# Optimization experiments

Hardware: AMD Instinct MI355X
Metric: run time of the kernel (lower is better)

The kernel has to match this reference:

```python
import jax, jax.numpy as jnp
import numpy as np

B, N, C_IN, C_OUT, R_IN, R_OUT, NUM_PSI, E = 4, 1024, 128, 256, 32, 32, 2, 65536


def psi(x, src, dst, W, b):
    # GIN-style GNN layer: aggregate neighbors via scatter-add, then linear+relu
    agg = jax.ops.segment_sum(x[src], dst, num_segments=x.shape[0])
    return jax.nn.relu((x + agg) @ W + b)


def setup_inputs() -> dict:
    key = jax.random.key(0)
    ks = jax.random.split(key, 12)
    inp = {
        'x_s': jax.random.normal(ks[0], (B * N, C_IN), jnp.float32),
        'edge_index_s': jax.random.randint(ks[1], (2, E), 0, B * N, jnp.int32),
        'x_t': jax.random.normal(ks[2], (B * N, C_IN), jnp.float32),
        'edge_index_t': jax.random.randint(ks[3], (2, E), 0, B * N, jnp.int32),
        'r': jax.random.normal(ks[4], (NUM_PSI, B, N, R_IN), jnp.float32),
        'W1': jax.random.normal(ks[5], (C_IN, C_OUT), jnp.float32) * (0.2 / np.sqrt(C_IN)),
        'b1': jnp.zeros((C_OUT,), jnp.float32),
        'Wp': jax.random.normal(ks[6], (NUM_PSI, R_IN, R_OUT), jnp.float32) * (1.0 / np.sqrt(R_IN)),
        'bp': jnp.zeros((NUM_PSI, R_OUT), jnp.float32),
        'Wm1': jax.random.normal(ks[7], (R_OUT, R_OUT), jnp.float32) * (1.0 / np.sqrt(R_OUT)),
        'bm1': jnp.zeros((R_OUT,), jnp.float32),
        'Wm2': jax.random.normal(ks[8], (R_OUT, 1), jnp.float32) * (1.0 / np.sqrt(R_OUT)),
        'bm2': jnp.zeros((1,), jnp.float32),
        'sum_weights': jnp.ones((NUM_PSI + 1,), jnp.float32),
    }
    return inp


def reference(x_s, edge_index_s, x_t, edge_index_t, r, W1, b1, Wp, bp, Wm1, bm1, Wm2, bm2, sum_weights):
    src_s, dst_s = edge_index_s[0], edge_index_s[1]
    src_t, dst_t = edge_index_t[0], edge_index_t[1]
    # psi_1 node embeddings, then dense-batch (equal-size graphs -> masks all true)
    h_s = psi(x_s, src_s, dst_s, W1, b1).reshape(B, N, C_OUT)
    h_t = psi(x_t, src_t, dst_t, W1, b1).reshape(B, N, C_OUT)
    S_hat = jnp.einsum('bsc,btc->bst', h_s, h_t)  # [B, N_s, N_t]
    S_0 = jax.nn.softmax(S_hat, axis=-1)
    S_stack = []
    for i in range(NUM_PSI):  # structurally distinct psi modules
        S = jax.nn.softmax(S_hat, axis=-1)
        r_s = r[i]  # [B, N, R_IN] random node indicators
        r_t = jnp.einsum('bst,bsr->btr', S, r_s)
        o_s = psi(r_s.reshape(B * N, R_IN), src_s, dst_s, Wp[i], bp[i]).reshape(B, N, R_OUT)
        o_t = psi(r_t.reshape(B * N, R_IN), src_t, dst_t, Wp[i], bp[i]).reshape(B, N, R_OUT)
        D = o_s[:, :, None, :] - o_t[:, None, :, :]  # [B, N_s, N_t, R_OUT]
        upd = (jax.nn.relu(D @ Wm1 + bm1) @ Wm2 + bm2)[..., 0]
        S_hat = S_hat + upd
        S_stack.append(jax.nn.softmax(S_hat, axis=-1))
    S_final = sum_weights[0] * S_0
    for i in range(NUM_PSI):
        S_final = S_final + sum_weights[i + 1] * S_stack[i]
    return jax.nn.softmax(S_final.reshape(B * N, N), axis=-1)
```

## Files before the change

### kernel.cpp

```cpp
#include <hip/hip_runtime.h>
#include <hip/hip_bf16.h>

#define NBATCH 4
#define NSEQ   1024
#define BNN    4096
#define CIN    128
#define COUT   256
#define RDIM   32
#define NEDGE  65536

__global__ void edge_hist(const int* __restrict__ ei_s, const int* __restrict__ ei_t,
                          int* __restrict__ cnt) {
    int gid = blockIdx.x * blockDim.x + threadIdx.x;
    int list = gid >> 16;
    int e = gid & (NEDGE - 1);
    const int* ei = list ? ei_t : ei_s;
    atomicAdd(&cnt[list * BNN + ei[NEDGE + e]], 1);
}

__global__ void edge_scan(const int* __restrict__ cnt, int* __restrict__ offs,
                          int* __restrict__ cursor) {
    __shared__ int sums[256];
    int list = blockIdx.x;
    int tid = threadIdx.x;
    int local[16];
    int s = 0;
#pragma unroll
    for (int k = 0; k < 16; k++) { local[k] = cnt[list * BNN + tid * 16 + k]; s += local[k]; }
    sums[tid] = s;
    __syncthreads();
    for (int off = 1; off < 256; off <<= 1) {
        int v = 0;
        if (tid >= off) v = sums[tid - off];
        __syncthreads();
        if (tid >= off) sums[tid] += v;
        __syncthreads();
    }
    int run = tid ? sums[tid - 1] : 0;
#pragma unroll
    for (int k = 0; k < 16; k++) {
        offs[list * (BNN + 1) + tid * 16 + k] = run;
        cursor[list * BNN + tid * 16 + k] = run;
        run += local[k];
    }
    if (tid == 255) offs[list * (BNN + 1) + BNN] = run;
}

__global__ void edge_place(const int* __restrict__ ei_s, const int* __restrict__ ei_t,
                           int* __restrict__ cursor, int* __restrict__ ssrc) {
    int gid = blockIdx.x * blockDim.x + threadIdx.x;
    int list = gid >> 16;
    int e = gid & (NEDGE - 1);
    const int* ei = list ? ei_t : ei_s;
    int dst = ei[NEDGE + e], src = ei[e];
    int p = atomicAdd(&cursor[list * BNN + dst], 1);
    ssrc[list * NEDGE + p] = src;
}

__global__ void gather_agg128(const float* __restrict__ x_s, const float* __restrict__ x_t,
                              const int* __restrict__ offs, const int* __restrict__ ssrc,
                              float* __restrict__ t_s, float* __restrict__ t_t) {
    int node = blockIdx.x & (BNN - 1);
    int list = blockIdx.x >> 12;
    const float* x = list ? x_t : x_s;
    float* t = list ? t_t : t_s;
    int c = threadIdx.x;
    int beg = offs[list * (BNN + 1) + node], end = offs[list * (BNN + 1) + node + 1];
    float acc = x[(size_t)node * CIN + c];
    for (int e = beg; e < end; e++)
        acc += x[(size_t)ssrc[list * NEDGE + e] * CIN + c];
    t[(size_t)node * CIN + c] = acc;
}

__global__ void gather_agg32(const float* __restrict__ rs, const float* __restrict__ rtin,
                             const int* __restrict__ offs, const int* __restrict__ ssrc,
                             float* __restrict__ trs, float* __restrict__ trt) {
    int list = blockIdx.y;
    int node = blockIdx.x * 8 + (threadIdx.x >> 5);
    int c = threadIdx.x & 31;
    const float* in = list ? rtin : rs;
    float* outp = list ? trt : trs;
    int beg = offs[list * (BNN + 1) + node], end = offs[list * (BNN + 1) + node + 1];
    float acc = in[(size_t)node * RDIM + c];
    for (int e = beg; e < end; e++)
        acc += in[(size_t)ssrc[list * NEDGE + e] * RDIM + c];
    outp[(size_t)node * RDIM + c] = acc;
}

__global__ void psi1_gemm(const float* __restrict__ t, const float* __restrict__ W1,
                          const float* __restrict__ b1, float* __restrict__ h) {
    __shared__ float rows[8][CIN];
    int r0 = blockIdx.x * 8;
    int tid = threadIdx.x;
    {
        int rr = tid >> 5, c4 = (tid & 31) << 2;
        *(float4*)&rows[rr][c4] = *(const float4*)(t + (size_t)(r0 + rr) * CIN + c4);
    }
    __syncthreads();
    float acc[8];
    float bias = b1[tid];
#pragma unroll
    for (int r = 0; r < 8; r++) acc[r] = bias;
    for (int k = 0; k < CIN; k++) {
        float w = W1[k * COUT + tid];
#pragma unroll
        for (int r = 0; r < 8; r++) acc[r] = fmaf(rows[r][k], w, acc[r]);
    }
#pragma unroll
    for (int r = 0; r < 8; r++)
        h[(size_t)(r0 + r) * COUT + tid] = fmaxf(acc[r], 0.f);
}

__global__ void shat_gemm(const float* __restrict__ hs, const float* __restrict__ ht,
                          float* __restrict__ Sh) {
    __shared__ float As[32][68];
    __shared__ float Bs[32][68];
    int b  = blockIdx.z;
    int s0 = blockIdx.y * 64, t0 = blockIdx.x * 64;
    const float* A  = hs + (size_t)b * NSEQ * COUT;
    const float* Bm = ht + (size_t)b * NSEQ * COUT;
    int tid = threadIdx.x;
    int tx = tid & 15, ty = tid >> 4;
    float acc[4][4] = {};
    for (int k0 = 0; k0 < COUT; k0 += 32) {
#pragma unroll
        for (int q = 0; q < 2; q++) {
            int lid = (tid << 1) + q;
            int row = lid >> 3, k4 = (lid & 7) << 2;
            float4 av = *(const float4*)(A + (size_t)(s0 + row) * COUT + k0 + k4);
            As[k4 + 0][row] = av.x; As[k4 + 1][row] = av.y;
            As[k4 + 2][row] = av.z; As[k4 + 3][row] = av.w;
            float4 bv = *(const float4*)(Bm + (size_t)(t0 + row) * COUT + k0 + k4);
            Bs[k4 + 0][row] = bv.x; Bs[k4 + 1][row] = bv.y;
            Bs[k4 + 2][row] = bv.z; Bs[k4 + 3][row] = bv.w;
        }
        __syncthreads();
#pragma unroll
        for (int k = 0; k < 32; k++) {
            float av[4], bv[4];
#pragma unroll
            for (int i = 0; i < 4; i++) av[i] = As[k][ty * 4 + i];
#pragma unroll
            for (int j = 0; j < 4; j++) bv[j] = Bs[k][tx * 4 + j];
#pragma unroll
            for (int i = 0; i < 4; i++)
#pragma unroll
                for (int j = 0; j < 4; j++)
                    acc[i][j] = fmaf(av[i], bv[j], acc[i][j]);
        }
        __syncthreads();
    }
#pragma unroll
    for (int i = 0; i < 4; i++) {
        float4 v = make_float4(acc[i][0], acc[i][1], acc[i][2], acc[i][3]);
        *(float4*)(Sh + ((size_t)b * NSEQ + s0 + ty * 4 + i) * NSEQ + t0 + tx * 4) = v;
    }
}

__global__ void softmax_acc(const float* __restrict__ Sh, float* __restrict__ S,
                            float* __restrict__ Sfin, const float* __restrict__ sw,
                            int widx, int init) {
    int row = blockIdx.x, tid = threadIdx.x;
    float4 v = *(const float4*)(Sh + (size_t)row * NSEQ + tid * 4);
    float m = fmaxf(fmaxf(v.x, v.y), fmaxf(v.z, v.w));
#pragma unroll
    for (int o = 32; o; o >>= 1) m = fmaxf(m, __shfl_xor(m, o));
    __shared__ float redm[4], reds[4];
    int wid = tid >> 6, lane = tid & 63;
    if (lane == 0) redm[wid] = m;
    __syncthreads();
    m = fmaxf(fmaxf(redm[0], redm[1]), fmaxf(redm[2], redm[3]));
    float4 e;
    e.x = __expf(v.x - m); e.y = __expf(v.y - m);
    e.z = __expf(v.z - m); e.w = __expf(v.w - m);
    float s = e.x + e.y + e.z + e.w;
#pragma unroll
    for (int o = 32; o; o >>= 1) s += __shfl_xor(s, o);
    if (lane == 0) reds[wid] = s;
    __syncthreads();
    s = reds[0] + reds[1] + reds[2] + reds[3];
    float inv = 1.0f / s;
    float4 sv = make_float4(e.x * inv, e.y * inv, e.z * inv, e.w * inv);
    *(float4*)(S + (size_t)row * NSEQ + tid * 4) = sv;
    float w = sw[widx];
    float* fp = Sfin + (size_t)row * NSEQ + tid * 4;
    float4 f;
    if (init) {
        f = make_float4(w * sv.x, w * sv.y, w * sv.z, w * sv.w);
    } else {
        float4 old = *(const float4*)fp;
        f = make_float4(fmaf(w, sv.x, old.x), fmaf(w, sv.y, old.y),
                        fmaf(w, sv.z, old.z), fmaf(w, sv.w, old.w));
    }
    *(float4*)fp = f;
}

__global__ void softmax_out(const float* __restrict__ Sf, float* __restrict__ out) {
    int row = blockIdx.x, tid = threadIdx.x;
    float4 v = *(const float4*)(Sf + (size_t)row * NSEQ + tid * 4);
    float m = fmaxf(fmaxf(v.x, v.y), fmaxf(v.z, v.w));
#pragma unroll
    for (int o = 32; o; o >>= 1) m = fmaxf(m, __shfl_xor(m, o));
    __shared__ float redm[4], reds[4];
    int wid = tid >> 6, lane = tid & 63;
    if (lane == 0) redm[wid] = m;
    __syncthreads();
    m = fmaxf(fmaxf(redm[0], redm[1]), fmaxf(redm[2], redm[3]));
    float4 e;
    e.x = __expf(v.x - m); e.y = __expf(v.y - m);
    e.z = __expf(v.z - m); e.w = __expf(v.w - m);
    float s = e.x + e.y + e.z + e.w;
#pragma unroll
    for (int o = 32; o; o >>= 1) s += __shfl_xor(s, o);
    if (lane == 0) reds[wid] = s;
    __syncthreads();
    s = reds[0] + reds[1] + reds[2] + reds[3];
    float inv = 1.0f / s;
    float4 sv = make_float4(e.x * inv, e.y * inv, e.z * inv, e.w * inv);
    *(float4*)(out + (size_t)row * NSEQ + tid * 4) = sv;
}

__global__ void rt_part(const float* __restrict__ S, const float* __restrict__ rs,
                        float* __restrict__ part) {
    __shared__ float rsld[64][33];
    int b = blockIdx.z, t0 = blockIdx.y * 128, s0 = blockIdx.x * 64;
    int tid = threadIdx.x;
#pragma unroll
    for (int q = 0; q < 2; q++) {
        int lid = (tid << 1) + q;
        int row = lid >> 3, c4 = (lid & 7) << 2;
        float4 v = *(const float4*)(rs + ((size_t)b * NSEQ + s0 + row) * RDIM + c4);
        rsld[row][c4] = v.x; rsld[row][c4 + 1] = v.y;
        rsld[row][c4 + 2] = v.z; rsld[row][c4 + 3] = v.w;
    }
    __syncthreads();
    int t = t0 + (tid & 127);
    int j0 = (tid >> 7) << 4;
    float acc[16] = {};
    const float* Sp = S + ((size_t)b * NSEQ + s0) * NSEQ + t;
#pragma unroll 8
    for (int s = 0; s < 64; s++) {
        float sv = Sp[(size_t)s * NSEQ];
#pragma unroll
        for (int j = 0; j < 16; j++) acc[j] = fmaf(sv, rsld[s][j0 + j], acc[j]);
    }
    float* pp = part + (((size_t)blockIdx.x * NBATCH + b) * NSEQ + t) * RDIM + j0;
#pragma unroll
    for (int j4 = 0; j4 < 16; j4 += 4)
        *(float4*)(pp + j4) = make_float4(acc[j4], acc[j4 + 1], acc[j4 + 2], acc[j4 + 3]);
}

__global__ void rt_reduce(const float* __restrict__ part, float* __restrict__ rt) {
    int i = blockIdx.x * blockDim.x + threadIdx.x;
    const float4* p = (const float4*)part + i;
    float4 a = make_float4(0.f, 0.f, 0.f, 0.f);
#pragma unroll
    for (int c = 0; c < 16; c++) {
        float4 v = p[(size_t)c * (BNN * RDIM / 4)];
        a.x += v.x; a.y += v.y; a.z += v.z; a.w += v.w;
    }
    ((float4*)rt)[i] = a;
}

__global__ void psi_r(const float* __restrict__ t_r, const float* __restrict__ Wp,
                      const float* __restrict__ bp, const float* __restrict__ Wm1,
                      const float* __restrict__ bm1, float* __restrict__ P, int add_bm1) {
    __shared__ float sWp[32 * 32], sWm1[32 * 32];
    __shared__ float srow[8][33], so[8][33];
    int tid = threadIdx.x;
#pragma unroll
    for (int q = 0; q < 4; q++) {
        sWp[tid + q * 256]  = Wp[tid + q * 256];
        sWm1[tid + q * 256] = Wm1[tid + q * 256];
    }
    int g = tid >> 5, j = tid & 31;
    int row = blockIdx.x * 8 + g;
    srow[g][j] = t_r[(size_t)row * RDIM + j];
    __syncthreads();
    float acc = bp[j];
#pragma unroll
    for (int k = 0; k < 32; k++) acc = fmaf(srow[g][k], sWp[k * 32 + j], acc);
    float o = fmaxf(acc, 0.f);
    so[g][j] = o;
    __syncthreads();
    float acc2 = add_bm1 ? bm1[j] : 0.f;
#pragma unroll
    for (int k = 0; k < 32; k++) acc2 = fmaf(so[g][k], sWm1[k * 32 + j], acc2);
    P[(size_t)row * RDIM + j] = acc2;
}

__global__ void upd_add(const float* __restrict__ Ps, const float* __restrict__ Pt,
                        const float* __restrict__ Wm2, const float* __restrict__ bm2p,
                        float* __restrict__ Sh) {
    __shared__ float sPs[64][33], sPt[64][33];
    __shared__ float swm[32];
    int b = blockIdx.z, s0 = blockIdx.y * 64, t0 = blockIdx.x * 64;
    int tid = threadIdx.x;
#pragma unroll
    for (int q = 0; q < 2; q++) {
        int lid = (tid << 1) + q, r = lid >> 3, c4 = (lid & 7) << 2;
        float4 a = *(const float4*)(Ps + ((size_t)b * NSEQ + s0 + r) * RDIM + c4);
        sPs[r][c4] = a.x; sPs[r][c4 + 1] = a.y; sPs[r][c4 + 2] = a.z; sPs[r][c4 + 3] = a.w;
        float4 c = *(const float4*)(Pt + ((size_t)b * NSEQ + t0 + r) * RDIM + c4);
        sPt[r][c4] = c.x; sPt[r][c4 + 1] = c.y; sPt[r][c4 + 2] = c.z; sPt[r][c4 + 3] = c.w;
    }
    if (tid < 32) swm[tid] = Wm2[tid];
    __syncthreads();
    float bm2 = bm2p[0];
    int tx = tid & 15, ty = tid >> 4;
    float acc[4][4] = {};
#pragma unroll
    for (int k = 0; k < 32; k++) {
        float w = swm[k];
        float ps[4], pt[4];
#pragma unroll
        for (int i = 0; i < 4; i++) ps[i] = sPs[ty * 4 + i][k];
#pragma unroll
        for (int j = 0; j < 4; j++) pt[j] = sPt[tx * 4 + j][k];
#pragma unroll
        for (int i = 0; i < 4; i++)
#pragma unroll
            for (int j = 0; j < 4; j++)
                acc[i][j] = fmaf(fmaxf(ps[i] - pt[j], 0.f), w, acc[i][j]);
    }
#pragma unroll
    for (int i = 0; i < 4; i++) {
        size_t base = ((size_t)b * NSEQ + s0 + ty * 4 + i) * NSEQ + t0 + tx * 4;
        float4 old = *(const float4*)(Sh + base);
        old.x += acc[i][0] + bm2; old.y += acc[i][1] + bm2;
        old.z += acc[i][2] + bm2; old.w += acc[i][3] + bm2;
        *(float4*)(Sh + base) = old;
    }
}

extern "C" void kernel_launch(void* const* d_in, const int* in_sizes, int n_in,
                              void* d_out, int out_size, void* d_ws, size_t ws_size,
                              hipStream_t stream) {
    const float* x_s  = (const float*)d_in[0];
    const int*   ei_s = (const int*)  d_in[1];
    const float* x_t  = (const float*)d_in[2];
    const int*   ei_t = (const int*)  d_in[3];
    const float* r    = (const float*)d_in[4];
    const float* W1   = (const float*)d_in[5];
    const float* b1   = (const float*)d_in[6];
    const float* Wp   = (const float*)d_in[7];
    const float* bp   = (const float*)d_in[8];
    const float* Wm1  = (const float*)d_in[9];
    const float* bm1  = (const float*)d_in[10];
    const float* Wm2  = (const float*)d_in[11];
    const float* bm2  = (const float*)d_in[12];
    const float* sw   = (const float*)d_in[13];
    float* out = (float*)d_out;

    float* ws = (float*)d_ws;
    float* t_s  = ws;  ws += (size_t)BNN * CIN;
    float* t_t  = ws;  ws += (size_t)BNN * CIN;
    float* h_s  = ws;  ws += (size_t)BNN * COUT;
    float* h_t  = ws;  ws += (size_t)BNN * COUT;
    float* Sh   = ws;  ws += (size_t)NBATCH * NSEQ * NSEQ;
    float* S    = ws;  ws += (size_t)NBATCH * NSEQ * NSEQ;
    float* Sfin = ws;  ws += (size_t)NBATCH * NSEQ * NSEQ;
    float* rt   = ws;  ws += (size_t)BNN * RDIM;
    float* trs  = ws;  ws += (size_t)BNN * RDIM;
    float* trt  = ws;  ws += (size_t)BNN * RDIM;
    float* Ps   = ws;  ws += (size_t)BNN * RDIM;
    float* Pt   = ws;  ws += (size_t)BNN * RDIM;
    int* icnt  = (int*)ws;
    int* ioffs = icnt  + 2 * BNN;
    int* icur  = ioffs + 2 * (BNN + 1);
    int* issrc = icur  + 2 * BNN;
    float* rtpart = h_s;

    hipMemsetAsync(icnt, 0, 2 * BNN * sizeof(int), stream);
    edge_hist <<<512, 256, 0, stream>>>(ei_s, ei_t, icnt);
    edge_scan <<<2, 256, 0, stream>>>(icnt, ioffs, icur);
    edge_place<<<512, 256, 0, stream>>>(ei_s, ei_t, icur, issrc);

    gather_agg128<<<8192, 128, 0, stream>>>(x_s, x_t, ioffs, issrc, t_s, t_t);
    psi1_gemm<<<512, 256, 0, stream>>>(t_s, W1, b1, h_s);
    psi1_gemm<<<512, 256, 0, stream>>>(t_t, W1, b1, h_t);
    shat_gemm<<<dim3(16, 16, 4), 256, 0, stream>>>(h_s, h_t, Sh);

    for (int i = 0; i < 2; i++) {
        softmax_acc<<<4096, 256, 0, stream>>>(Sh, S, Sfin, sw, i, i == 0 ? 1 : 0);
        rt_part<<<dim3(16, 8, 4), 256, 0, stream>>>(S, r + (size_t)i * BNN * RDIM, rtpart);
        rt_reduce<<<128, 256, 0, stream>>>(rtpart, rt);
        gather_agg32<<<dim3(512, 2), 256, 0, stream>>>(r + (size_t)i * BNN * RDIM, rt,
                                                       ioffs, issrc, trs, trt);
        psi_r<<<512, 256, 0, stream>>>(trs, Wp + i * RDIM * RDIM, bp + i * RDIM,
                                       Wm1, bm1, Ps, 1);
        psi_r<<<512, 256, 0, stream>>>(trt, Wp + i * RDIM * RDIM, bp + i * RDIM,
                                       Wm1, bm1, Pt, 0);
        upd_add<<<dim3(16, 16, 4), 256, 0, stream>>>(Ps, Pt, Wm2, bm2, Sh);
    }
    softmax_acc<<<4096, 256, 0, stream>>>(Sh, S, Sfin, sw, 2, 0);
    softmax_out<<<4096, 256, 0, stream>>>(Sfin, out);
}
```

Baseline: 246.6 us.

## Fuse softmax passes, drop S matrix, retile S_hat GEMM, merge psi launches

Several changes land together. Neighbor gathers are batched through shared memory. The two psi1 and psi_r launches are merged into single launches, and the S_hat GEMM moves to 128x128 tiles with an 8x8 register block and register prefetch. The softmax probability matrix S is no longer stored: row max and inverse-sum statistics are saved and rt_part recomputes the exponentials, and the last softmax_acc is fused with the output softmax. This removes a 16MB write and read per iteration plus one full pass, at the cost of extra exp work and higher register pressure in the GEMM.

New measurement: 223.5 us. 1.1x faster.

```diff
diff --git a/kernel.cpp b/kernel.cpp
--- a/kernel.cpp
+++ b/kernel.cpp
@@ -60,6 +60,7 @@
 __global__ void gather_agg128(const float* __restrict__ x_s, const float* __restrict__ x_t,
                               const int* __restrict__ offs, const int* __restrict__ ssrc,
                               float* __restrict__ t_s, float* __restrict__ t_t) {
+    __shared__ int sl[128];
     int node = blockIdx.x & (BNN - 1);
     int list = blockIdx.x >> 12;
     const float* x = list ? x_t : x_s;
@@ -67,8 +68,19 @@
     int c = threadIdx.x;
     int beg = offs[list * (BNN + 1) + node], end = offs[list * (BNN + 1) + node + 1];
     float acc = x[(size_t)node * CIN + c];
-    for (int e = beg; e < end; e++)
-        acc += x[(size_t)ssrc[list * NEDGE + e] * CIN + c];
+    for (int base = beg; base < end; base += 128) {
+        int cnt = min(128, end - base);
+        __syncthreads();
+        if (c < cnt) sl[c] = ssrc[list * NEDGE + base + c];
+        __syncthreads();
+        int e = 0;
+        for (; e + 4 <= cnt; e += 4) {
+            int n0 = sl[e], n1 = sl[e + 1], n2 = sl[e + 2], n3 = sl[e + 3];
+            acc += x[(size_t)n0 * CIN + c] + x[(size_t)n1 * CIN + c]
+                 + x[(size_t)n2 * CIN + c] + x[(size_t)n3 * CIN + c];
+        }
+        for (; e < cnt; e++) acc += x[(size_t)sl[e] * CIN + c];
+    }
     t[(size_t)node * CIN + c] = acc;
 }
 
@@ -87,10 +99,14 @@
     outp[(size_t)node * RDIM + c] = acc;
 }
 
-__global__ void psi1_gemm(const float* __restrict__ t, const float* __restrict__ W1,
-                          const float* __restrict__ b1, float* __restrict__ h) {
+__global__ void psi1_gemm(const float* __restrict__ t_s, const float* __restrict__ t_t,
+                          const float* __restrict__ W1, const float* __restrict__ b1,
+                          float* __restrict__ h_s, float* __restrict__ h_t) {
     __shared__ float rows[8][CIN];
-    int r0 = blockIdx.x * 8;
+    int half = blockIdx.x >> 9;
+    const float* t = half ? t_t : t_s;
+    float* h = half ? h_t : h_s;
+    int r0 = (blockIdx.x & 511) * 8;
     int tid = threadIdx.x;
     {
         int rr = tid >> 5, c4 = (tid & 31) << 2;
@@ -111,55 +127,66 @@
         h[(size_t)(r0 + r) * COUT + tid] = fmaxf(acc[r], 0.f);
 }
 
-__global__ void shat_gemm(const float* __restrict__ hs, const float* __restrict__ ht,
-                          float* __restrict__ Sh) {
-    __shared__ float As[32][68];
-    __shared__ float Bs[32][68];
+__global__ __launch_bounds__(256) void shat_gemm(const float* __restrict__ hs,
+                                                 const float* __restrict__ ht,
+                                                 float* __restrict__ Sh) {
+    __shared__ float As[16][132];
+    __shared__ float Bs[16][132];
     int b  = blockIdx.z;
-    int s0 = blockIdx.y * 64, t0 = blockIdx.x * 64;
+    int s0 = blockIdx.y * 128, t0 = blockIdx.x * 128;
     const float* A  = hs + (size_t)b * NSEQ * COUT;
     const float* Bm = ht + (size_t)b * NSEQ * COUT;
     int tid = threadIdx.x;
     int tx = tid & 15, ty = tid >> 4;
-    float acc[4][4] = {};
-    for (int k0 = 0; k0 < COUT; k0 += 32) {
-#pragma unroll
-        for (int q = 0; q < 2; q++) {
-            int lid = (tid << 1) + q;
-            int row = lid >> 3, k4 = (lid & 7) << 2;
-            float4 av = *(const float4*)(A + (size_t)(s0 + row) * COUT + k0 + k4);
-            As[k4 + 0][row] = av.x; As[k4 + 1][row] = av.y;
-            As[k4 + 2][row] = av.z; As[k4 + 3][row] = av.w;
-            float4 bv = *(const float4*)(Bm + (size_t)(t0 + row) * COUT + k0 + k4);
-            Bs[k4 + 0][row] = bv.x; Bs[k4 + 1][row] = bv.y;
-            Bs[k4 + 2][row] = bv.z; Bs[k4 + 3][row] = bv.w;
+    int lr = tid >> 1;
+    int lk = (tid & 1) * 8;
+    const float* Ap = A  + (size_t)(s0 + lr) * COUT + lk;
+    const float* Bp = Bm + (size_t)(t0 + lr) * COUT + lk;
+    float4 a0 = *(const float4*)(Ap);
+    float4 a1 = *(const float4*)(Ap + 4);
+    float4 b0 = *(const float4*)(Bp);
+    float4 b1 = *(const float4*)(Bp + 4);
+    float acc[8][8] = {};
+    for (int kp = 0; kp < 16; kp++) {
+        __syncthreads();
+        As[lk + 0][lr] = a0.x; As[lk + 1][lr] = a0.y; As[lk + 2][lr] = a0.z; As[lk + 3][lr] = a0.w;
+        As[lk + 4][lr] = a1.x; As[lk + 5][lr] = a1.y; As[lk + 6][lr] = a1.z; As[lk + 7][lr] = a1.w;
+        Bs[lk + 0][lr] = b0.x; Bs[lk + 1][lr] = b0.y; Bs[lk + 2][lr] = b0.z; Bs[lk + 3][lr] = b0.w;
+        Bs[lk + 4][lr] = b1.x; Bs[lk + 5][lr] = b1.y; Bs[lk + 6][lr] = b1.z; Bs[lk + 7][lr] = b1.w;
+        __syncthreads();
+        if (kp < 15) {
+            a0 = *(const float4*)(Ap + (kp + 1) * 16);
+            a1 = *(const float4*)(Ap + (kp + 1) * 16 + 4);
+            b0 = *(const float4*)(Bp + (kp + 1) * 16);
+            b1 = *(const float4*)(Bp + (kp + 1) * 16 + 4);
         }
-        __syncthreads();
-#pragma unroll
-        for (int k = 0; k < 32; k++) {
-            float av[4], bv[4];
-#pragma unroll
-            for (int i = 0; i < 4; i++) av[i] = As[k][ty * 4 + i];
-#pragma unroll
-            for (int j = 0; j < 4; j++) bv[j] = Bs[k][tx * 4 + j];
-#pragma unroll
-            for (int i = 0; i < 4; i++)
-#pragma unroll
-                for (int j = 0; j < 4; j++)
+#pragma unroll
+        for (int k = 0; k < 16; k++) {
+            float av[8], bv[8];
+            *(float4*)&av[0] = *(const float4*)&As[k][ty * 8];
+            *(float4*)&av[4] = *(const float4*)&As[k][ty * 8 + 4];
+            *(float4*)&bv[0] = *(const float4*)&Bs[k][tx * 8];
+            *(float4*)&bv[4] = *(const float4*)&Bs[k][tx * 8 + 4];
+#pragma unroll
+            for (int i = 0; i < 8; i++)
+#pragma unroll
+                for (int j = 0; j < 8; j++)
                     acc[i][j] = fmaf(av[i], bv[j], acc[i][j]);
         }
-        __syncthreads();
-    }
-#pragma unroll
-    for (int i = 0; i < 4; i++) {
-        float4 v = make_float4(acc[i][0], acc[i][1], acc[i][2], acc[i][3]);
-        *(float4*)(Sh + ((size_t)b * NSEQ + s0 + ty * 4 + i) * NSEQ + t0 + tx * 4) = v;
-    }
-}
-
-__global__ void softmax_acc(const float* __restrict__ Sh, float* __restrict__ S,
-                            float* __restrict__ Sfin, const float* __restrict__ sw,
-                            int widx, int init) {
+    }
+#pragma unroll
+    for (int i = 0; i < 8; i++) {
+#pragma unroll
+        for (int j4 = 0; j4 < 8; j4 += 4) {
+            float4 v = make_float4(acc[i][j4], acc[i][j4 + 1], acc[i][j4 + 2], acc[i][j4 + 3]);
+            *(float4*)(Sh + ((size_t)b * NSEQ + s0 + ty * 8 + i) * NSEQ + t0 + tx * 8 + j4) = v;
+        }
+    }
+}
+
+__global__ void softmax_acc2(const float* __restrict__ Sh, float* __restrict__ Sfin,
+                             const float* __restrict__ sw, float* __restrict__ mstat,
+                             float* __restrict__ istat, int widx, int init) {
     int row = blockIdx.x, tid = threadIdx.x;
     float4 v = *(const float4*)(Sh + (size_t)row * NSEQ + tid * 4);
     float m = fmaxf(fmaxf(v.x, v.y), fmaxf(v.z, v.w));
@@ -180,29 +207,29 @@
     __syncthreads();
     s = reds[0] + reds[1] + reds[2] + reds[3];
     float inv = 1.0f / s;
-    float4 sv = make_float4(e.x * inv, e.y * inv, e.z * inv, e.w * inv);
-    *(float4*)(S + (size_t)row * NSEQ + tid * 4) = sv;
-    float w = sw[widx];
+    float w = sw[widx] * inv;
     float* fp = Sfin + (size_t)row * NSEQ + tid * 4;
     float4 f;
     if (init) {
-        f = make_float4(w * sv.x, w * sv.y, w * sv.z, w * sv.w);
+        f = make_float4(w * e.x, w * e.y, w * e.z, w * e.w);
     } else {
         float4 old = *(const float4*)fp;
-        f = make_float4(fmaf(w, sv.x, old.x), fmaf(w, sv.y, old.y),
-                        fmaf(w, sv.z, old.z), fmaf(w, sv.w, old.w));
+        f = make_float4(fmaf(w, e.x, old.x), fmaf(w, e.y, old.y),
+                        fmaf(w, e.z, old.z), fmaf(w, e.w, old.w));
     }
     *(float4*)fp = f;
-}
-
-__global__ void softmax_out(const float* __restrict__ Sf, float* __restrict__ out) {
+    if (tid == 0) { mstat[row] = m; istat[row] = inv; }
+}
+
+__global__ void softmax_final(const float* __restrict__ Sh, const float* __restrict__ Sfin,
+                              const float* __restrict__ sw, float* __restrict__ out) {
     int row = blockIdx.x, tid = threadIdx.x;
-    float4 v = *(const float4*)(Sf + (size_t)row * NSEQ + tid * 4);
+    __shared__ float redm[4], reds[4], redm2[4], reds2[4];
+    int wid = tid >> 6, lane = tid & 63;
+    float4 v = *(const float4*)(Sh + (size_t)row * NSEQ + tid * 4);
     float m = fmaxf(fmaxf(v.x, v.y), fmaxf(v.z, v.w));
 #pragma unroll
     for (int o = 32; o; o >>= 1) m = fmaxf(m, __shfl_xor(m, o));
-    __shared__ float redm[4], reds[4];
-    int wid = tid >> 6, lane = tid & 63;
     if (lane == 0) redm[wid] = m;
     __syncthreads();
     m = fmaxf(fmaxf(redm[0], redm[1]), fmaxf(redm[2], redm[3]));
@@ -215,34 +242,57 @@
     if (lane == 0) reds[wid] = s;
     __syncthreads();
     s = reds[0] + reds[1] + reds[2] + reds[3];
-    float inv = 1.0f / s;
-    float4 sv = make_float4(e.x * inv, e.y * inv, e.z * inv, e.w * inv);
+    float w = sw[2] / s;
+    float4 old = *(const float4*)(Sfin + (size_t)row * NSEQ + tid * 4);
+    float4 f = make_float4(fmaf(w, e.x, old.x), fmaf(w, e.y, old.y),
+                           fmaf(w, e.z, old.z), fmaf(w, e.w, old.w));
+    float m2 = fmaxf(fmaxf(f.x, f.y), fmaxf(f.z, f.w));
+#pragma unroll
+    for (int o = 32; o; o >>= 1) m2 = fmaxf(m2, __shfl_xor(m2, o));
+    if (lane == 0) redm2[wid] = m2;
+    __syncthreads();
+    m2 = fmaxf(fmaxf(redm2[0], redm2[1]), fmaxf(redm2[2], redm2[3]));
+    float4 e2;
+    e2.x = __expf(f.x - m2); e2.y = __expf(f.y - m2);
+    e2.z = __expf(f.z - m2); e2.w = __expf(f.w - m2);
+    float s2 = e2.x + e2.y + e2.z + e2.w;
+#pragma unroll
+    for (int o = 32; o; o >>= 1) s2 += __shfl_xor(s2, o);
+    if (lane == 0) reds2[wid] = s2;
+    __syncthreads();
+    s2 = reds2[0] + reds2[1] + reds2[2] + reds2[3];
+    float inv2 = 1.0f / s2;
+    float4 sv = make_float4(e2.x * inv2, e2.y * inv2, e2.z * inv2, e2.w * inv2);
     *(float4*)(out + (size_t)row * NSEQ + tid * 4) = sv;
 }
 
-__global__ void rt_part(const float* __restrict__ S, const float* __restrict__ rs,
+__global__ void rt_part(const float* __restrict__ Sh, const float* __restrict__ mstat,
+                        const float* __restrict__ istat, const float* __restrict__ rs,
                         float* __restrict__ part) {
     __shared__ float rsld[64][33];
+    __shared__ float ml[64], il[64];
     int b = blockIdx.z, t0 = blockIdx.y * 128, s0 = blockIdx.x * 64;
     int tid = threadIdx.x;
+    if (tid < 64) ml[tid] = mstat[b * NSEQ + s0 + tid];
+    else if (tid < 128) il[tid - 64] = istat[b * NSEQ + s0 + tid - 64];
 #pragma unroll
     for (int q = 0; q < 2; q++) {
         int lid = (tid << 1) + q;
-        int row = lid >> 3, c4 = (lid & 7) << 2;
-        float4 v = *(const float4*)(rs + ((size_t)b * NSEQ + s0 + row) * RDIM + c4);
-        rsld[row][c4] = v.x; rsld[row][c4 + 1] = v.y;
-        rsld[row][c4 + 2] = v.z; rsld[row][c4 + 3] = v.w;
+        int srow = lid >> 3, c4 = (lid & 7) << 2;
+        float4 v = *(const float4*)(rs + ((size_t)b * NSEQ + s0 + srow) * RDIM + c4);
+        rsld[srow][c4] = v.x; rsld[srow][c4 + 1] = v.y;
+        rsld[srow][c4 + 2] = v.z; rsld[srow][c4 + 3] = v.w;
     }
     __syncthreads();
     int t = t0 + (tid & 127);
     int j0 = (tid >> 7) << 4;
     float acc[16] = {};
-    const float* Sp = S + ((size_t)b * NSEQ + s0) * NSEQ + t;
+    const float* Sp = Sh + ((size_t)b * NSEQ + s0) * NSEQ + t;
 #pragma unroll 8
     for (int s = 0; s < 64; s++) {
-        float sv = Sp[(size_t)s * NSEQ];
-#pragma unroll
-        for (int j = 0; j < 16; j++) acc[j] = fmaf(sv, rsld[s][j0 + j], acc[j]);
+        float p = __expf(Sp[(size_t)s * NSEQ] - ml[s]) * il[s];
+#pragma unroll
+        for (int j = 0; j < 16; j++) acc[j] = fmaf(p, rsld[s][j0 + j], acc[j]);
     }
     float* pp = part + (((size_t)blockIdx.x * NBATCH + b) * NSEQ + t) * RDIM + j0;
 #pragma unroll
@@ -262,11 +312,15 @@
     ((float4*)rt)[i] = a;
 }
 
-__global__ void psi_r(const float* __restrict__ t_r, const float* __restrict__ Wp,
-                      const float* __restrict__ bp, const float* __restrict__ Wm1,
-                      const float* __restrict__ bm1, float* __restrict__ P, int add_bm1) {
+__global__ void psi_r(const float* __restrict__ trs, const float* __restrict__ trt,
+                      const float* __restrict__ Wp, const float* __restrict__ bp,
+                      const float* __restrict__ Wm1, const float* __restrict__ bm1,
+                      float* __restrict__ Ps, float* __restrict__ Pt) {
     __shared__ float sWp[32 * 32], sWm1[32 * 32];
     __shared__ float srow[8][33], so[8][33];
+    int which = blockIdx.y;
+    const float* t_r = which ? trt : trs;
+    float* P = which ? Pt : Ps;
     int tid = threadIdx.x;
 #pragma unroll
     for (int q = 0; q < 4; q++) {
@@ -283,7 +337,7 @@
     float o = fmaxf(acc, 0.f);
     so[g][j] = o;
     __syncthreads();
-    float acc2 = add_bm1 ? bm1[j] : 0.f;
+    float acc2 = which ? 0.f : bm1[j];
 #pragma unroll
     for (int k = 0; k < 32; k++) acc2 = fmaf(so[g][k], sWm1[k * 32 + j], acc2);
     P[(size_t)row * RDIM + j] = acc2;
@@ -298,11 +352,11 @@
     int tid = threadIdx.x;
 #pragma unroll
     for (int q = 0; q < 2; q++) {
-        int lid = (tid << 1) + q, r = lid >> 3, c4 = (lid & 7) << 2;
-        float4 a = *(const float4*)(Ps + ((size_t)b * NSEQ + s0 + r) * RDIM + c4);
-        sPs[r][c4] = a.x; sPs[r][c4 + 1] = a.y; sPs[r][c4 + 2] = a.z; sPs[r][c4 + 3] = a.w;
-        float4 c = *(const float4*)(Pt + ((size_t)b * NSEQ + t0 + r) * RDIM + c4);
-        sPt[r][c4] = c.x; sPt[r][c4 + 1] = c.y; sPt[r][c4 + 2] = c.z; sPt[r][c4 + 3] = c.w;
+        int lid = (tid << 1) + q, rr = lid >> 3, c4 = (lid & 7) << 2;
+        float4 a = *(const float4*)(Ps + ((size_t)b * NSEQ + s0 + rr) * RDIM + c4);
+        sPs[rr][c4] = a.x; sPs[rr][c4 + 1] = a.y; sPs[rr][c4 + 2] = a.z; sPs[rr][c4 + 3] = a.w;
+        float4 c = *(const float4*)(Pt + ((size_t)b * NSEQ + t0 + rr) * RDIM + c4);
+        sPt[rr][c4] = c.x; sPt[rr][c4 + 1] = c.y; sPt[rr][c4 + 2] = c.z; sPt[rr][c4 + 3] = c.w;
     }
     if (tid < 32) swm[tid] = Wm2[tid];
     __syncthreads();
@@ -358,8 +412,9 @@
     float* h_s  = ws;  ws += (size_t)BNN * COUT;
     float* h_t  = ws;  ws += (size_t)BNN * COUT;
     float* Sh   = ws;  ws += (size_t)NBATCH * NSEQ * NSEQ;
-    float* S    = ws;  ws += (size_t)NBATCH * NSEQ * NSEQ;
     float* Sfin = ws;  ws += (size_t)NBATCH * NSEQ * NSEQ;
+    float* mstat = ws; ws += BNN;
+    float* istat = ws; ws += BNN;
     float* rt   = ws;  ws += (size_t)BNN * RDIM;
     float* trs  = ws;  ws += (size_t)BNN * RDIM;
     float* trt  = ws;  ws += (size_t)BNN * RDIM;
@@ -377,22 +432,19 @@
     edge_place<<<512, 256, 0, stream>>>(ei_s, ei_t, icur, issrc);
 
     gather_agg128<<<8192, 128, 0, stream>>>(x_s, x_t, ioffs, issrc, t_s, t_t);
-    psi1_gemm<<<512, 256, 0, stream>>>(t_s, W1, b1, h_s);
-    psi1_gemm<<<512, 256, 0, stream>>>(t_t, W1, b1, h_t);
-    shat_gemm<<<dim3(16, 16, 4), 256, 0, stream>>>(h_s, h_t, Sh);
+    psi1_gemm<<<1024, 256, 0, stream>>>(t_s, t_t, W1, b1, h_s, h_t);
+    shat_gemm<<<dim3(8, 8, 4), 256, 0, stream>>>(h_s, h_t, Sh);
 
     for (int i = 0; i < 2; i++) {
-        softmax_acc<<<4096, 256, 0, stream>>>(Sh, S, Sfin, sw, i, i == 0 ? 1 : 0);
-        rt_part<<<dim3(16, 8, 4), 256, 0, stream>>>(S, r + (size_t)i * BNN * RDIM, rtpart);
+        softmax_acc2<<<4096, 256, 0, stream>>>(Sh, Sfin, sw, mstat, istat, i, i == 0 ? 1 : 0);
+        rt_part<<<dim3(16, 8, 4), 256, 0, stream>>>(Sh, mstat, istat,
+                                                    r + (size_t)i * BNN * RDIM, rtpart);
         rt_reduce<<<128, 256, 0, stream>>>(rtpart, rt);
         gather_agg32<<<dim3(512, 2), 256, 0, stream>>>(r + (size_t)i * BNN * RDIM, rt,
                                                        ioffs, issrc, trs, trt);
-        psi_r<<<512, 256, 0, stream>>>(trs, Wp + i * RDIM * RDIM, bp + i * RDIM,
-                                       Wm1, bm1, Ps, 1);
-        psi_r<<<512, 256, 0, stream>>>(trt, Wp + i * RDIM * RDIM, bp + i * RDIM,
-                                       Wm1, bm1, Pt, 0);
+        psi_r<<<dim3(512, 2), 256, 0, stream>>>(trs, trt, Wp + i * RDIM * RDIM,
+                                                bp + i * RDIM, Wm1, bm1, Ps, Pt);
         upd_add<<<dim3(16, 16, 4), 256, 0, stream>>>(Ps, Pt, Wm2, bm2, Sh);
     }
-    softmax_acc<<<4096, 256, 0, stream>>>(Sh, S, Sfin, sw, 2, 0);
-    softmax_out<<<4096, 256, 0, stream>>>(Sfin, out);
-}
+    softmax_final<<<4096, 256, 0, stream>>>(Sh, Sfin, sw, out);
+}
```
